# Kernel optimization log

Measured on AMD Instinct MI355X. Metric: run time of the kernel, lower is better.

Reference implementation:

```python
import jax, jax.numpy as jnp
import numpy as np

B, F_NODES, E = 1024, 128, 1024   # graphs, nodes/graph, edges/graph
H, HEADS = 128, 4
HD = H // HEADS


def setup_inputs() -> dict:
    key = jax.random.key(0)
    ks = jax.random.split(key, 24)
    f32 = jnp.float32
    n = jax.random.normal
    d = {
        "x": n(ks[0], (B, F_NODES), f32),
        "edge_index": jax.random.randint(ks[1], (2, E), 0, F_NODES, dtype=jnp.int32),
        # input projection Linear(1, H)
        "w_in": n(ks[2], (1, H), f32) * 0.5,
        "b_in": n(ks[3], (H,), f32) * 0.02,
        # GAT layer 0: heads=4, concat=True, per-head dim HD
        "gat0_w": n(ks[4], (H, H), f32) * (1.0 / np.sqrt(H)),
        "gat0_as": n(ks[5], (HEADS, HD), f32) * 0.1,
        "gat0_ad": n(ks[6], (HEADS, HD), f32) * 0.1,
        "gat0_b": n(ks[7], (H,), f32) * 0.02,
        "bn0_g": 1.0 + 0.1 * n(ks[8], (H,), f32),
        "bn0_b": 0.1 * n(ks[9], (H,), f32),
        "bn0_m": 0.1 * n(ks[10], (H,), f32),
        "bn0_v": 1.0 + 0.1 * jax.random.uniform(ks[11], (H,), f32),
        # GAT layer 1: heads=1, concat=False
        "gat1_w": n(ks[12], (H, H), f32) * (1.0 / np.sqrt(H)),
        "gat1_as": n(ks[13], (1, H), f32) * 0.1,
        "gat1_ad": n(ks[14], (1, H), f32) * 0.1,
        "gat1_b": n(ks[15], (H,), f32) * 0.02,
        "bn1_g": 1.0 + 0.1 * n(ks[16], (H,), f32),
        "bn1_b": 0.1 * n(ks[17], (H,), f32),
        "bn1_m": 0.1 * n(ks[18], (H,), f32),
        "bn1_v": 1.0 + 0.1 * jax.random.uniform(ks[19], (H,), f32),
        # classifier MLP H -> H//2 -> 1
        "w1": n(ks[20], (H, H // 2), f32) * (1.0 / np.sqrt(H)),
        "b1": n(ks[21], (H // 2,), f32) * 0.02,
        "w2": n(ks[22], (H // 2, 1), f32) * (1.0 / np.sqrt(H // 2)),
        "b2": n(ks[23], (1,), f32) * 0.02,
    }
    return d


def _gat(h, src, dst, N, W, a_s, a_d, b, concat):
    # PyG GATConv (shared lin for src/dst, leaky_relu slope 0.2, softmax over dst)
    heads, hd = a_s.shape
    xh = (h @ W).reshape(N, heads, hd)                      # [N, heads, hd]
    e = jax.nn.leaky_relu(
        jnp.sum(xh * a_s[None], -1)[src] + jnp.sum(xh * a_d[None], -1)[dst],
        0.2,
    )                                                        # [Etot, heads]
    m = jax.ops.segment_max(e, dst, num_segments=N)
    ex = jnp.exp(e - m[dst])
    s = jax.ops.segment_sum(ex, dst, num_segments=N)
    alpha = ex / s[dst]
    out = jax.ops.segment_sum(xh[src] * alpha[..., None], dst, num_segments=N)
    out = out.reshape(N, heads * hd) if concat else out[:, 0]
    return out + b


def _bn(h, g, b, m, v):
    return (h - m) / jnp.sqrt(v + 1e-5) * g + b


def reference(x, edge_index, w_in, b_in,
              gat0_w, gat0_as, gat0_ad, gat0_b, bn0_g, bn0_b, bn0_m, bn0_v,
              gat1_w, gat1_as, gat1_ad, gat1_b, bn1_g, bn1_b, bn1_m, bn1_v,
              w1, b1, w2, b2):
    Bsz, Fn = x.shape
    N = Bsz * Fn
    h = jax.nn.relu(x.reshape(N, 1) @ w_in + b_in)           # [N, H]
    # replicate per-graph edges with node offsets, then add self loops
    offs = jnp.arange(Bsz, dtype=edge_index.dtype) * Fn
    eib = (edge_index[:, None, :] + offs[None, :, None]).reshape(2, -1)
    loops = jnp.arange(N, dtype=edge_index.dtype)
    src = jnp.concatenate([eib[0], loops])
    dst = jnp.concatenate([eib[1], loops])
    h = _gat(h, src, dst, N, gat0_w, gat0_as, gat0_ad, gat0_b, True)
    h = jax.nn.relu(_bn(h, bn0_g, bn0_b, bn0_m, bn0_v))
    h = _gat(h, src, dst, N, gat1_w, gat1_as, gat1_ad, gat1_b, False)
    h = jax.nn.relu(_bn(h, bn1_g, bn1_b, bn1_m, bn1_v))
    # global mean pool (each graph has exactly Fn nodes)
    hp = h.reshape(Bsz, Fn, -1).mean(axis=1)                 # [B, H]
    z = jax.nn.relu(hp @ w1 + b1)
    return z @ w2 + b2                                       # [B, 1]
```

## Files before the change

kernel.cpp:

```cpp
#include <hip/hip_runtime.h>

#define FN   128
#define HDIM 128
#define NH   4
#define HSZ  32
#define EB   1024
#define ET   1152
#define RSW  132

typedef __attribute__((ext_vector_type(8))) short bf16x8;
typedef __attribute__((ext_vector_type(4))) float f32x4;
typedef unsigned int u32;
typedef unsigned short u16;

union U8 { bf16x8 v; u32 u[4]; };

__device__ __forceinline__ u32 pack_hl(float v) {
  const u32 u = __float_as_uint(v);
  const u32 hib = u & 0xFFFF0000u;
  const float lo = v - __uint_as_float(hib);
  return hib | (__float_as_uint(lo) >> 16);
}
__device__ __forceinline__ float unpack_val(u32 p) {
  return __uint_as_float(p & 0xFFFF0000u) + __uint_as_float(p << 16);
}
__device__ __forceinline__ float lrelu(float v) {
  return (v > 0.f) ? v : 0.2f * v;
}

__device__ __forceinline__ void unpack_frag(const u32* __restrict__ q,
                                            bf16x8& hi, bf16x8& lo)
{
  const uint4 p0 = *(const uint4*)(q);
  const uint4 p1 = *(const uint4*)(q + 4);
  U8 H, L;
  H.u[0] = (p0.x >> 16) | (p0.y & 0xFFFF0000u);
  L.u[0] = (p0.x & 0xFFFFu) | (p0.y << 16);
  H.u[1] = (p0.z >> 16) | (p0.w & 0xFFFF0000u);
  L.u[1] = (p0.z & 0xFFFFu) | (p0.w << 16);
  H.u[2] = (p1.x >> 16) | (p1.y & 0xFFFF0000u);
  L.u[2] = (p1.x & 0xFFFFu) | (p1.y << 16);
  H.u[3] = (p1.z >> 16) | (p1.w & 0xFFFF0000u);
  L.u[3] = (p1.z & 0xFFFFu) | (p1.w << 16);
  hi = H.v; lo = L.v;
}

__global__ __launch_bounds__(256) void prep_w_kernel(
    const float* __restrict__ g0w, const float* __restrict__ g1w,
    u16* __restrict__ wf)
{
  const int idx = blockIdx.x * 256 + threadIdx.x;
  const int layer = idx >> 14;
  const int r = idx & 16383;
  const int c  = r >> 11;
  const int kc = (r >> 9) & 3;
  const int l  = (r >> 3) & 63;
  const int j  = r & 7;
  const int k = kc * 32 + (l >> 4) * 8 + j;
  const int n = c * 16 + (l & 15);
  const float* W = layer ? g1w : g0w;
  const float v = W[k * HDIM + n];
  const u32 u = __float_as_uint(v);
  const u32 hib = u & 0xFFFF0000u;
  const float lo = v - __uint_as_float(hib);
  wf[layer * 32768 + r]         = (u16)(u >> 16);
  wf[layer * 32768 + 16384 + r] = (u16)(__float_as_uint(lo) >> 16);
}

__device__ __forceinline__ void mfma_gemm_acc(const u32* __restrict__ F,
                                              const u16* __restrict__ wf,
                                              int lw, int lane, f32x4 acc[4][2])
{
  const int cg = lw & 3, rh = lw >> 2;
  const int m = lane & 15, quad = lane >> 4;

  #pragma unroll
  for (int s = 0; s < 4; ++s)
    #pragma unroll
    for (int ct = 0; ct < 2; ++ct) acc[s][ct] = (f32x4){0.f, 0.f, 0.f, 0.f};

  const u16* bbase = wf + (cg * 8) * 512 + lane * 8;

  #pragma unroll
  for (int kc = 0; kc < 4; ++kc) {
    bf16x8 bhi[2], blo[2];
    #pragma unroll
    for (int ct = 0; ct < 2; ++ct) {
      const u16* bp = bbase + ct * 2048 + kc * 512;
      bhi[ct] = *(const bf16x8*)bp;
      blo[ct] = *(const bf16x8*)(bp + 16384);
    }
    #pragma unroll
    for (int s = 0; s < 4; ++s) {
      const u32* ap = F + (rh * 64 + s * 16 + m) * RSW + quad * 8 + kc * 32;
      bf16x8 ahi, alo;
      unpack_frag(ap, ahi, alo);
      #pragma unroll
      for (int ct = 0; ct < 2; ++ct) {
        acc[s][ct] = __builtin_amdgcn_mfma_f32_16x16x32_bf16(ahi, bhi[ct], acc[s][ct], 0, 0, 0);
        acc[s][ct] = __builtin_amdgcn_mfma_f32_16x16x32_bf16(alo, bhi[ct], acc[s][ct], 0, 0, 0);
        acc[s][ct] = __builtin_amdgcn_mfma_f32_16x16x32_bf16(ahi, blo[ct], acc[s][ct], 0, 0, 0);
      }
    }
  }
}

__device__ __forceinline__ void store_acc(float* __restrict__ sg, int lw,
                                          int lane, const f32x4 acc[4][2])
{
  const int cg = lw & 3, rh = lw >> 2;
  const int m = lane & 15, quad = lane >> 4;
  #pragma unroll
  for (int s = 0; s < 4; ++s) {
    const int row0 = rh * 64 + s * 16 + quad * 4;
    #pragma unroll
    for (int ct = 0; ct < 2; ++ct)
      #pragma unroll
      for (int r = 0; r < 4; ++r)
        sg[(row0 + r) * RSW + cg * 32 + ct * 16 + m] = acc[s][ct][r];
  }
}

__global__ __launch_bounds__(1024) void gnn_fused_kernel(
    const float* __restrict__ x, const int* __restrict__ ei,
    const float* __restrict__ w_in, const float* __restrict__ b_in,
    const float* __restrict__ g0as, const float* __restrict__ g0ad,
    const float* __restrict__ g0b,
    const float* __restrict__ bn0g, const float* __restrict__ bn0b,
    const float* __restrict__ bn0m, const float* __restrict__ bn0v,
    const float* __restrict__ g1as, const float* __restrict__ g1ad,
    const float* __restrict__ g1b,
    const float* __restrict__ bn1g, const float* __restrict__ bn1b,
    const float* __restrict__ bn1m, const float* __restrict__ bn1v,
    const float* __restrict__ w1, const float* __restrict__ b1,
    const float* __restrict__ w2, const float* __restrict__ b2,
    const u16* __restrict__ wf,
    float* __restrict__ out)
{
  __shared__ u32   Fb[2 * FN * RSW];
  __shared__ int   s_src[ET];
  __shared__ int   s_rp[FN + 1];
  __shared__ float s_scr[3072];
  __shared__ float s_bn[512];

  const int t = threadIdx.x;
  const int b = blockIdx.x;
  const int g = t >> 9;
  const int u = t & 511;
  const int lane = t & 63;
  const int lw = (t >> 6) & 7;
  u32*   F    = Fb + g * (FN * RSW);
  float* s_es = s_scr + g * 1536;
  float* s_ed = s_es + 512;
  float* s_rs = s_es + 1024;
  f32x4 acc[4][2];

  int* s_deg  = (int*)s_scr;
  int* s_fill = s_deg + 128;
  const int e_dst = ei[EB + t];
  const int e_src = ei[t];
  if (t < 2 * FN) s_deg[t] = 0;
  __syncthreads();
  atomicAdd(&s_deg[e_dst], 1);

  {
    const int j = u & 127, q = u >> 7;
    const float wv = w_in[j], bv = b_in[j];
    const size_t xb = (size_t)(b * 2 + g) * FN;
    for (int n = q * 32; n < q * 32 + 32; ++n) {
      const float v = fmaxf(fmaf(x[xb + n], wv, bv), 0.f);
      F[n * RSW + j] = pack_hl(v);
    }
  }
  __syncthreads();
  if (t < 64) {
    const int v0 = s_deg[2 * t] + 1, v1 = s_deg[2 * t + 1] + 1;
    const int p = v0 + v1;
    int sc = p;
    #pragma unroll
    for (int off = 1; off < 64; off <<= 1) {
      const int o = __shfl_up(sc, off, 64);
      if (t >= off) sc += o;
    }
    s_rp[2 * t] = sc - p;
    s_rp[2 * t + 1] = sc - v1;
    if (t == 63) s_rp[128] = sc;
  } else if (t >= 512 && t < 768) {
    const int layer = (t >> 7) & 1;
    const int col = t & 127;
    const float bb = layer ? g1b[col]  : g0b[col];
    const float bm = layer ? bn1m[col] : bn0m[col];
    const float bv = layer ? bn1v[col] : bn0v[col];
    const float bg = layer ? bn1g[col] : bn0g[col];
    const float bt = layer ? bn1b[col] : bn0b[col];
    const float q = bg * rsqrtf(bv + 1e-5f);
    s_bn[layer * 256 + col] = q;
    s_bn[layer * 256 + 128 + col] = (bb - bm) * q + bt;
  }
  __syncthreads();
  {
    const int p = s_rp[e_dst] + atomicAdd(&s_fill[e_dst], 1);
    s_src[p] = e_src | (e_dst << 8);
  }
  if (t < FN) s_src[s_rp[t + 1] - 1] = t | (t << 8);
  __syncthreads();

  mfma_gemm_acc(F, wf, lw, lane, acc);
  __syncthreads();
  store_acc((float*)F, lw, lane, acc);
  __syncthreads();

  {
    const int hh = u >> 7, n = u & 127;
    const float* row = (const float*)F + n * RSW + hh * HSZ;
    float accs = 0.f, accd = 0.f;
    #pragma unroll
    for (int s = 0; s < 8; ++s) {
      const int d = ((n + s) & 7) * 4;
      const float4 v  = *(const float4*)(row + d);
      const float4 as = *(const float4*)(g0as + hh * HSZ + d);
      const float4 ad = *(const float4*)(g0ad + hh * HSZ + d);
      accs += v.x*as.x + v.y*as.y + v.z*as.z + v.w*as.w;
      accd += v.x*ad.x + v.y*ad.y + v.z*ad.z + v.w*ad.w;
    }
    s_es[hh * 128 + n] = accs;
    s_ed[hh * 128 + n] = accd;
  }
  __syncthreads();

  {
    const int n = u & 127, hh = u >> 7;
    const int cb = hh * HSZ;
    const float* Ff = (const float*)F;
    const int e0 = s_rp[n], e1 = s_rp[n + 1];
    const float edv = s_ed[hh * 128 + n];
    const float* esb = s_es + hh * 128;
    float sum = 0.f;
    for (int e = e0; e < e1; ++e)
      sum += __expf(lrelu(esb[s_src[e] & 127] + edv));
    const float rsv = 1.f / sum;
    float4 a[8];
    #pragma unroll
    for (int i = 0; i < 8; ++i) a[i] = make_float4(0.f, 0.f, 0.f, 0.f);
    for (int e = e0; e < e1; ++e) {
      const int s = s_src[e] & 127;
      const float al = __expf(lrelu(esb[s] + edv));
      const float* rp_ = Ff + s * RSW + cb;
      #pragma unroll
      for (int i = 0; i < 8; ++i) {
        const float4 vv = *(const float4*)(rp_ + i * 4);
        a[i].x = fmaf(al, vv.x, a[i].x); a[i].y = fmaf(al, vv.y, a[i].y);
        a[i].z = fmaf(al, vv.z, a[i].z); a[i].w = fmaf(al, vv.w, a[i].w);
      }
    }
    __syncthreads();
    #pragma unroll
    for (int i = 0; i < 8; ++i) {
      const int col = cb + i * 4;
      const float4 q = *(const float4*)&s_bn[col];
      const float4 r = *(const float4*)&s_bn[128 + col];
      uint4 p;
      p.x = pack_hl(fmaxf(fmaf(a[i].x * rsv, q.x, r.x), 0.f));
      p.y = pack_hl(fmaxf(fmaf(a[i].y * rsv, q.y, r.y), 0.f));
      p.z = pack_hl(fmaxf(fmaf(a[i].z * rsv, q.z, r.z), 0.f));
      p.w = pack_hl(fmaxf(fmaf(a[i].w * rsv, q.w, r.w), 0.f));
      *(uint4*)(F + n * RSW + col) = p;
    }
  }
  __syncthreads();

  mfma_gemm_acc(F, wf + 32768, lw, lane, acc);
  __syncthreads();
  store_acc((float*)F, lw, lane, acc);
  __syncthreads();

  {
    const int n = u >> 2, c = u & 3;
    const float* row = (const float*)F + n * RSW + c * 32;
    float accs = 0.f, accd = 0.f;
    #pragma unroll
    for (int i = 0; i < 8; ++i) {
      const int d = i * 4;
      const float4 v  = *(const float4*)(row + d);
      const float4 as = *(const float4*)(g1as + c * 32 + d);
      const float4 ad = *(const float4*)(g1ad + c * 32 + d);
      accs += v.x*as.x + v.y*as.y + v.z*as.z + v.w*as.w;
      accd += v.x*ad.x + v.y*ad.y + v.z*ad.z + v.w*ad.w;
    }
    s_es[u] = accs;
    s_ed[u] = accd;
  }
  __syncthreads();
  if (u < 128) {
    const float* pe = s_es + u * 4;
    const float* pd = s_ed + u * 4;
    s_rs[u]       = pe[0] + pe[1] + pe[2] + pe[3];
    s_rs[128 + u] = pd[0] + pd[1] + pd[2] + pd[3];
  }
  __syncthreads();

  {
    const int n = u & 127, cg = u >> 7;
    const int cb = cg * HSZ;
    const float* Ff = (const float*)F;
    const int e0 = s_rp[n], e1 = s_rp[n + 1];
    const float edv = s_rs[128 + n];
    float sum = 0.f;
    for (int e = e0; e < e1; ++e)
      sum += __expf(lrelu(s_rs[s_src[e] & 127] + edv));
    const float rsv = 1.f / sum;
    float4 a[8];
    #pragma unroll
    for (int i = 0; i < 8; ++i) a[i] = make_float4(0.f, 0.f, 0.f, 0.f);
    for (int e = e0; e < e1; ++e) {
      const int s = s_src[e] & 127;
      const float al = __expf(lrelu(s_rs[s] + edv));
      const float* rp_ = Ff + s * RSW + cb;
      #pragma unroll
      for (int i = 0; i < 8; ++i) {
        const float4 vv = *(const float4*)(rp_ + i * 4);
        a[i].x = fmaf(al, vv.x, a[i].x); a[i].y = fmaf(al, vv.y, a[i].y);
        a[i].z = fmaf(al, vv.z, a[i].z); a[i].w = fmaf(al, vv.w, a[i].w);
      }
    }
    __syncthreads();
    #pragma unroll
    for (int i = 0; i < 8; ++i) {
      const int col = cb + i * 4;
      const float4 q = *(const float4*)&s_bn[256 + col];
      const float4 r = *(const float4*)&s_bn[384 + col];
      uint4 p;
      p.x = __float_as_uint(fmaxf(fmaf(a[i].x * rsv, q.x, r.x), 0.f));
      p.y = __float_as_uint(fmaxf(fmaf(a[i].y * rsv, q.y, r.y), 0.f));
      p.z = __float_as_uint(fmaxf(fmaf(a[i].z * rsv, q.z, r.z), 0.f));
      p.w = __float_as_uint(fmaxf(fmaf(a[i].w * rsv, q.w, r.w), 0.f));
      *(uint4*)(F + n * RSW + col) = p;
    }
  }
  __syncthreads();

  {
    const int j = u & 127, q = u >> 7;
    float p = 0.f;
    for (int n = q * 32; n < q * 32 + 32; ++n)
      p += __uint_as_float(F[n * RSW + j]);
    s_es[q * 128 + j] = p;
  }
  __syncthreads();
  if (u < 128) {
    s_ed[u] = (s_es[u] + s_es[u + 128] + s_es[u + 256] + s_es[u + 384])
              * (1.f / 128.f);
  }
  __syncthreads();
  {
    const int j = u & 63, part = u >> 6;
    float a = 0.f;
    #pragma unroll
    for (int k = part * 16; k < part * 16 + 16; ++k)
      a = fmaf(s_ed[k], w1[k * 64 + j], a);
    s_rs[part * 64 + j] = a;
  }
  __syncthreads();
  if (u < 64) {
    float a = b1[u];
    #pragma unroll
    for (int p = 0; p < 8; ++p) a += s_rs[p * 64 + u];
    a = fmaxf(a, 0.f);
    float v = a * w2[u];
    #pragma unroll
    for (int off = 32; off > 0; off >>= 1) v += __shfl_down(v, off, 64);
    if (u == 0) out[b * 2 + g] = v + b2[0];
  }
}

extern "C" void kernel_launch(void* const* d_in, const int* in_sizes, int n_in,
                              void* d_out, int out_size, void* d_ws, size_t ws_size,
                              hipStream_t stream)
{
  const float* x    = (const float*)d_in[0];
  const int*   ei   = (const int*)d_in[1];
  const float* w_in = (const float*)d_in[2];
  const float* b_in = (const float*)d_in[3];
  const float* g0w  = (const float*)d_in[4];
  const float* g0as = (const float*)d_in[5];
  const float* g0ad = (const float*)d_in[6];
  const float* g0b  = (const float*)d_in[7];
  const float* bn0g = (const float*)d_in[8];
  const float* bn0b = (const float*)d_in[9];
  const float* bn0m = (const float*)d_in[10];
  const float* bn0v = (const float*)d_in[11];
  const float* g1w  = (const float*)d_in[12];
  const float* g1as = (const float*)d_in[13];
  const float* g1ad = (const float*)d_in[14];
  const float* g1b  = (const float*)d_in[15];
  const float* bn1g = (const float*)d_in[16];
  const float* bn1b = (const float*)d_in[17];
  const float* bn1m = (const float*)d_in[18];
  const float* bn1v = (const float*)d_in[19];
  const float* w1   = (const float*)d_in[20];
  const float* b1   = (const float*)d_in[21];
  const float* w2   = (const float*)d_in[22];
  const float* b2   = (const float*)d_in[23];

  u16* wf = (u16*)d_ws;

  prep_w_kernel<<<128, 256, 0, stream>>>(g0w, g1w, wf);
  gnn_fused_kernel<<<512, 1024, 0, stream>>>(x, ei, w_in, b_in,
      g0as, g0ad, g0b, bn0g, bn0b, bn0m, bn0v,
      g1as, g1ad, g1b, bn1g, bn1b, bn1m, bn1v,
      w1, b1, w2, b2, wf, (float*)d_out);
}
```

Measured before the change: 191.3 us.

## Precompute shared CSR once, switch to one graph per 512-thread block, degree-sort nodes

The per-block CSR build (degree atomics, scan, scatter) moves into a single-block prep kernel, since every graph shares the same edge_index. The fused kernel now handles one graph per 512-thread block instead of two per 1024-thread block, and loads the CSR from the workspace. Aggregation threads are assigned nodes in descending-degree order to even out per-wave work. The separate softmax-sum pass is folded into the aggregation loop. The trade-off is an extra tiny serial kernel launch and twice as many blocks, each with less parallel slack.

```diff
diff --git a/kernel.cpp b/kernel.cpp
--- a/kernel.cpp
+++ b/kernel.cpp
@@ -67,6 +67,41 @@
   wf[layer * 32768 + 16384 + r] = (u16)(__float_as_uint(lo) >> 16);
 }
 
+__global__ __launch_bounds__(256) void prep_csr_kernel(
+    const int* __restrict__ ei, int* __restrict__ csr)
+{
+  __shared__ int deg[FN], rp[FN + 1], fill[FN];
+  const int t = threadIdx.x;
+  if (t < FN) { deg[t] = 0; fill[t] = 0; }
+  __syncthreads();
+  for (int e = t; e < EB; e += 256) atomicAdd(&deg[ei[EB + e]], 1);
+  __syncthreads();
+  if (t == 0) {
+    int acc = 0;
+    for (int n = 0; n < FN; ++n) { rp[n] = acc; acc += deg[n] + 1; }
+    rp[FN] = acc;
+  }
+  __syncthreads();
+  if (t < FN) {
+    const int dn = deg[t];
+    int rk = 0;
+    for (int m = 0; m < FN; ++m) {
+      const int dm = deg[m];
+      rk += (dm > dn) || (dm == dn && m < t);
+    }
+    csr[ET + FN + 1 + rk] = t;
+    csr[ET + t] = rp[t];
+    if (t == 0) csr[ET + FN] = rp[FN];
+  }
+  __syncthreads();
+  for (int e = t; e < EB; e += 256) {
+    const int d = ei[EB + e], s = ei[e];
+    const int p = rp[d] + atomicAdd(&fill[d], 1);
+    csr[p] = s | (d << 8);
+  }
+  if (t < FN) csr[rp[t] + deg[t]] = t | (t << 8);
+}
+
 __device__ __forceinline__ void mfma_gemm_acc(const u32* __restrict__ F,
                                               const u16* __restrict__ wf,
                                               int lw, int lane, f32x4 acc[4][2])
@@ -121,8 +156,8 @@
   }
 }
 
-__global__ __launch_bounds__(1024) void gnn_fused_kernel(
-    const float* __restrict__ x, const int* __restrict__ ei,
+__global__ __launch_bounds__(512) void gnn_fused_kernel(
+    const float* __restrict__ x,
     const float* __restrict__ w_in, const float* __restrict__ b_in,
     const float* __restrict__ g0as, const float* __restrict__ g0ad,
     const float* __restrict__ g0b,
@@ -134,59 +169,30 @@
     const float* __restrict__ bn1m, const float* __restrict__ bn1v,
     const float* __restrict__ w1, const float* __restrict__ b1,
     const float* __restrict__ w2, const float* __restrict__ b2,
-    const u16* __restrict__ wf,
+    const u16* __restrict__ wf, const int* __restrict__ csr,
     float* __restrict__ out)
 {
-  __shared__ u32   Fb[2 * FN * RSW];
+  __shared__ u32   F[FN * RSW];
   __shared__ int   s_src[ET];
   __shared__ int   s_rp[FN + 1];
-  __shared__ float s_scr[3072];
+  __shared__ int   s_perm[FN];
+  __shared__ float s_scr[1280];
   __shared__ float s_bn[512];
 
   const int t = threadIdx.x;
-  const int b = blockIdx.x;
-  const int g = t >> 9;
-  const int u = t & 511;
+  const int gid = blockIdx.x;
   const int lane = t & 63;
-  const int lw = (t >> 6) & 7;
-  u32*   F    = Fb + g * (FN * RSW);
-  float* s_es = s_scr + g * 1536;
-  float* s_ed = s_es + 512;
-  float* s_rs = s_es + 1024;
+  const int lw = t >> 6;
+  float* s_es = s_scr;
+  float* s_ed = s_scr + 512;
+  float* s_rs = s_scr + 1024;
   f32x4 acc[4][2];
 
-  int* s_deg  = (int*)s_scr;
-  int* s_fill = s_deg + 128;
-  const int e_dst = ei[EB + t];
-  const int e_src = ei[t];
-  if (t < 2 * FN) s_deg[t] = 0;
-  __syncthreads();
-  atomicAdd(&s_deg[e_dst], 1);
-
-  {
-    const int j = u & 127, q = u >> 7;
-    const float wv = w_in[j], bv = b_in[j];
-    const size_t xb = (size_t)(b * 2 + g) * FN;
-    for (int n = q * 32; n < q * 32 + 32; ++n) {
-      const float v = fmaxf(fmaf(x[xb + n], wv, bv), 0.f);
-      F[n * RSW + j] = pack_hl(v);
-    }
-  }
-  __syncthreads();
-  if (t < 64) {
-    const int v0 = s_deg[2 * t] + 1, v1 = s_deg[2 * t + 1] + 1;
-    const int p = v0 + v1;
-    int sc = p;
-    #pragma unroll
-    for (int off = 1; off < 64; off <<= 1) {
-      const int o = __shfl_up(sc, off, 64);
-      if (t >= off) sc += o;
-    }
-    s_rp[2 * t] = sc - p;
-    s_rp[2 * t + 1] = sc - v1;
-    if (t == 63) s_rp[128] = sc;
-  } else if (t >= 512 && t < 768) {
-    const int layer = (t >> 7) & 1;
+  for (int e = t; e < ET; e += 512) s_src[e] = csr[e];
+  if (t < FN + 1) s_rp[t] = csr[ET + t];
+  if (t < FN)     s_perm[t] = csr[ET + FN + 1 + t];
+  if (t < 256) {
+    const int layer = t >> 7;
     const int col = t & 127;
     const float bb = layer ? g1b[col]  : g0b[col];
     const float bm = layer ? bn1m[col] : bn0m[col];
@@ -197,12 +203,15 @@
     s_bn[layer * 256 + col] = q;
     s_bn[layer * 256 + 128 + col] = (bb - bm) * q + bt;
   }
-  __syncthreads();
-  {
-    const int p = s_rp[e_dst] + atomicAdd(&s_fill[e_dst], 1);
-    s_src[p] = e_src | (e_dst << 8);
-  }
-  if (t < FN) s_src[s_rp[t + 1] - 1] = t | (t << 8);
+  {
+    const int j = t & 127, q = t >> 7;
+    const float wv = w_in[j], bv = b_in[j];
+    const size_t xb = (size_t)gid * FN;
+    for (int n = q * 32; n < q * 32 + 32; ++n) {
+      const float v = fmaxf(fmaf(x[xb + n], wv, bv), 0.f);
+      F[n * RSW + j] = pack_hl(v);
+    }
+  }
   __syncthreads();
 
   mfma_gemm_acc(F, wf, lw, lane, acc);
@@ -211,7 +220,7 @@
   __syncthreads();
 
   {
-    const int hh = u >> 7, n = u & 127;
+    const int hh = t >> 7, n = t & 127;
     const float* row = (const float*)F + n * RSW + hh * HSZ;
     float accs = 0.f, accd = 0.f;
     #pragma unroll
@@ -229,22 +238,21 @@
   __syncthreads();
 
   {
-    const int n = u & 127, hh = u >> 7;
+    const int slot = t & 127, hh = t >> 7;
+    const int n = s_perm[slot];
     const int cb = hh * HSZ;
     const float* Ff = (const float*)F;
     const int e0 = s_rp[n], e1 = s_rp[n + 1];
     const float edv = s_ed[hh * 128 + n];
     const float* esb = s_es + hh * 128;
     float sum = 0.f;
-    for (int e = e0; e < e1; ++e)
-      sum += __expf(lrelu(esb[s_src[e] & 127] + edv));
-    const float rsv = 1.f / sum;
     float4 a[8];
     #pragma unroll
     for (int i = 0; i < 8; ++i) a[i] = make_float4(0.f, 0.f, 0.f, 0.f);
     for (int e = e0; e < e1; ++e) {
       const int s = s_src[e] & 127;
       const float al = __expf(lrelu(esb[s] + edv));
+      sum += al;
       const float* rp_ = Ff + s * RSW + cb;
       #pragma unroll
       for (int i = 0; i < 8; ++i) {
@@ -253,6 +261,7 @@
         a[i].z = fmaf(al, vv.z, a[i].z); a[i].w = fmaf(al, vv.w, a[i].w);
       }
     }
+    const float rsv = 1.f / sum;
     __syncthreads();
     #pragma unroll
     for (int i = 0; i < 8; ++i) {
@@ -275,7 +284,7 @@
   __syncthreads();
 
   {
-    const int n = u >> 2, c = u & 3;
+    const int n = t >> 2, c = t & 3;
     const float* row = (const float*)F + n * RSW + c * 32;
     float accs = 0.f, accd = 0.f;
     #pragma unroll
@@ -287,34 +296,33 @@
       accs += v.x*as.x + v.y*as.y + v.z*as.z + v.w*as.w;
       accd += v.x*ad.x + v.y*ad.y + v.z*ad.z + v.w*ad.w;
     }
-    s_es[u] = accs;
-    s_ed[u] = accd;
-  }
-  __syncthreads();
-  if (u < 128) {
-    const float* pe = s_es + u * 4;
-    const float* pd = s_ed + u * 4;
-    s_rs[u]       = pe[0] + pe[1] + pe[2] + pe[3];
-    s_rs[128 + u] = pd[0] + pd[1] + pd[2] + pd[3];
-  }
-  __syncthreads();
-
-  {
-    const int n = u & 127, cg = u >> 7;
+    s_es[t] = accs;
+    s_ed[t] = accd;
+  }
+  __syncthreads();
+  if (t < 128) {
+    const float* pe = s_es + t * 4;
+    const float* pd = s_ed + t * 4;
+    s_rs[t]       = pe[0] + pe[1] + pe[2] + pe[3];
+    s_rs[128 + t] = pd[0] + pd[1] + pd[2] + pd[3];
+  }
+  __syncthreads();
+
+  {
+    const int slot = t & 127, cg = t >> 7;
+    const int n = s_perm[slot];
     const int cb = cg * HSZ;
     const float* Ff = (const float*)F;
     const int e0 = s_rp[n], e1 = s_rp[n + 1];
     const float edv = s_rs[128 + n];
     float sum = 0.f;
-    for (int e = e0; e < e1; ++e)
-      sum += __expf(lrelu(s_rs[s_src[e] & 127] + edv));
-    const float rsv = 1.f / sum;
     float4 a[8];
     #pragma unroll
     for (int i = 0; i < 8; ++i) a[i] = make_float4(0.f, 0.f, 0.f, 0.f);
     for (int e = e0; e < e1; ++e) {
       const int s = s_src[e] & 127;
       const float al = __expf(lrelu(s_rs[s] + edv));
+      sum += al;
       const float* rp_ = Ff + s * RSW + cb;
       #pragma unroll
       for (int i = 0; i < 8; ++i) {
@@ -323,6 +331,7 @@
         a[i].z = fmaf(al, vv.z, a[i].z); a[i].w = fmaf(al, vv.w, a[i].w);
       }
     }
+    const float rsv = 1.f / sum;
     __syncthreads();
     #pragma unroll
     for (int i = 0; i < 8; ++i) {
@@ -340,36 +349,36 @@
   __syncthreads();
 
   {
-    const int j = u & 127, q = u >> 7;
+    const int j = t & 127, q = t >> 7;
     float p = 0.f;
     for (int n = q * 32; n < q * 32 + 32; ++n)
       p += __uint_as_float(F[n * RSW + j]);
     s_es[q * 128 + j] = p;
   }
   __syncthreads();
-  if (u < 128) {
-    s_ed[u] = (s_es[u] + s_es[u + 128] + s_es[u + 256] + s_es[u + 384])
+  if (t < 128) {
+    s_ed[t] = (s_es[t] + s_es[t + 128] + s_es[t + 256] + s_es[t + 384])
               * (1.f / 128.f);
   }
   __syncthreads();
   {
-    const int j = u & 63, part = u >> 6;
+    const int j = t & 63, part = t >> 6;
     float a = 0.f;
     #pragma unroll
     for (int k = part * 16; k < part * 16 + 16; ++k)
       a = fmaf(s_ed[k], w1[k * 64 + j], a);
-    s_rs[part * 64 + j] = a;
-  }
-  __syncthreads();
-  if (u < 64) {
-    float a = b1[u];
-    #pragma unroll
-    for (int p = 0; p < 8; ++p) a += s_rs[p * 64 + u];
+    s_es[part * 64 + j] = a;
+  }
+  __syncthreads();
+  if (t < 64) {
+    float a = b1[t];
+    #pragma unroll
+    for (int p = 0; p < 8; ++p) a += s_es[p * 64 + t];
     a = fmaxf(a, 0.f);
-    float v = a * w2[u];
+    float v = a * w2[t];
     #pragma unroll
     for (int off = 32; off > 0; off >>= 1) v += __shfl_down(v, off, 64);
-    if (u == 0) out[b * 2 + g] = v + b2[0];
+    if (t == 0) out[gid] = v + b2[0];
   }
 }
 
@@ -402,11 +411,13 @@
   const float* w2   = (const float*)d_in[22];
   const float* b2   = (const float*)d_in[23];
 
-  u16* wf = (u16*)d_ws;
+  u16* wf  = (u16*)d_ws;
+  int* csr = (int*)((char*)d_ws + 131072);
 
   prep_w_kernel<<<128, 256, 0, stream>>>(g0w, g1w, wf);
-  gnn_fused_kernel<<<512, 1024, 0, stream>>>(x, ei, w_in, b_in,
+  prep_csr_kernel<<<1, 256, 0, stream>>>(ei, csr);
+  gnn_fused_kernel<<<1024, 512, 0, stream>>>(x, w_in, b_in,
       g0as, g0ad, g0b, bn0g, bn0b, bn0m, bn0v,
       g1as, g1ad, g1b, bn1g, bn1b, bn1m, bn1v,
-      w1, b1, w2, b2, wf, (float*)d_out);
-}
+      w1, b1, w2, b2, wf, csr, (float*)d_out);
+}
```

Measured after the change: 188.2 us. No clear change (-1.6%).
